# Performance work log

Hardware: AMD Instinct MI355X
Metric: run time of the kernel (lower is better)

## Reference

```python
import jax, jax.numpy as jnp
import numpy as np

D = 128      # embed_dim
H = 8        # num_heads
HD = D // H  # head_dim
TANH_CLIP = 10.0
B, N = 256, 2000


def setup_inputs() -> dict:
    key = jax.random.key(0)
    ks = jax.random.split(key, 16)
    node_embedding = jax.random.normal(ks[0], (B, N, D), jnp.float32)
    graph_embed = jax.random.normal(ks[1], (B, D), jnp.float32)
    h_last = jax.random.normal(ks[2], (B, D), jnp.float32)
    h_first = jax.random.normal(ks[3], (B, D), jnp.float32)
    visited_mask = jax.random.randint(ks[4], (B, N), 0, 2) > 0
    visited_mask = visited_mask.at[:, 0].set(False)  # keep >=1 valid key per row
    s = 1.0 / np.sqrt(D)
    v_l = jax.random.normal(ks[5], (1, D), jnp.float32)
    v_f = jax.random.normal(ks[6], (1, D), jnp.float32)
    w_q = jax.random.uniform(ks[7], (D, 3 * D), jnp.float32, -s, s)   # Linear(3D->D) weight [out,in]
    w_k = jax.random.uniform(ks[8], (D, D), jnp.float32, -s, s)
    w_v = jax.random.uniform(ks[9], (D, D), jnp.float32, -s, s)
    in_proj_w = jax.random.uniform(ks[10], (3 * D, D), jnp.float32, -s, s)  # MHA packed qkv proj
    in_proj_b = jnp.zeros((3 * D,), jnp.float32)
    out_w = jax.random.uniform(ks[11], (D, D), jnp.float32, -s, s)    # MHA out_proj weight
    out_b = jnp.zeros((D,), jnp.float32)
    return {
        'node_embedding': node_embedding, 'graph_embed': graph_embed,
        'h_last': h_last, 'h_first': h_first, 'visited_mask': visited_mask, 't': 1,
        'v_l': v_l, 'v_f': v_f, 'w_q': w_q, 'w_k': w_k, 'w_v': w_v,
        'in_proj_w': in_proj_w, 'in_proj_b': in_proj_b, 'out_w': out_w, 'out_b': out_b,
    }


def reference(node_embedding, graph_embed, h_last, h_first, visited_mask, t,
              v_l, v_f, w_q, w_k, w_v, in_proj_w, in_proj_b, out_w, out_b):
    b, n, d = node_embedding.shape
    if t == 0:  # static python int
        h_last = jnp.broadcast_to(v_l, (b, d))
        h_first = jnp.broadcast_to(v_f, (b, d))
    context = jnp.concatenate([graph_embed, h_last, h_first], axis=-1)  # [B,3D]

    q0 = context @ w_q.T                        # [B,D]
    k0 = jnp.einsum('bnd,ed->bne', node_embedding, w_k)  # [B,N,D]
    v0 = jnp.einsum('bnd,ed->bne', node_embedding, w_v)

    # nn.MultiheadAttention internal projections (packed in_proj)
    wq_i, wk_i, wv_i = in_proj_w[:d], in_proj_w[d:2 * d], in_proj_w[2 * d:]
    bq, bk, bv = in_proj_b[:d], in_proj_b[d:2 * d], in_proj_b[2 * d:]
    qp = (q0 @ wq_i.T + bq).reshape(b, H, HD)                 # single query
    kp = (jnp.einsum('bnd,ed->bne', k0, wk_i) + bk).reshape(b, n, H, HD)
    vp = (jnp.einsum('bnd,ed->bne', v0, wv_i) + bv).reshape(b, n, H, HD)

    scores = jnp.einsum('bhe,bnhe->bhn', qp, kp) / np.sqrt(HD)  # [B,H,N]
    scores = jnp.where(visited_mask[:, None, :], -jnp.inf, scores)
    attn = jax.nn.softmax(scores, axis=-1)
    ctx = jnp.einsum('bhn,bnhe->bhe', attn, vp).reshape(b, d)
    h_c_new = ctx @ out_w.T + out_b                           # [B,D]

    logits = jnp.einsum('bd,bnd->bn', h_c_new, k0) / np.sqrt(d)
    logits = TANH_CLIP * jnp.tanh(logits)
    logits = jnp.where(visited_mask, -jnp.inf, logits)
    probs = jax.nn.softmax(logits, axis=-1)
    return probs, logits
```

## Files before the change

kernel.cpp:

```cpp
#include <hip/hip_runtime.h>
#include <math.h>

#define DD 128
#define HH 8
#define BB 256
#define NNODES 2000
#define NSL 16
#define SLEN 125
#define CH 8
#define NCH 16
#define TANH_CLIPF 10.0f
#define NEG_BIG -1e30f

#define WS_WKP   0
#define WS_WVP   16384
#define WS_QH    32768
#define WS_QB    294912
#define WS_PM    296960
#define WS_PS    329728
#define WS_PACC  362496
#define WS_G     4556800
#define WS_LL    4589568

__global__ void prep_weights(const float* __restrict__ w_k, const float* __restrict__ w_v,
                             const float* __restrict__ in_proj_w, float* __restrict__ ws) {
    int idx = blockIdx.x * 256 + threadIdx.x;
    int mat = idx >> 14;
    int e = (idx >> 7) & 127;
    int d = idx & 127;
    const float* A  = in_proj_w + (mat ? 2 * DD * DD : DD * DD) + e * DD;
    const float* Bm = mat ? w_v : w_k;
    float acc = 0.f;
    for (int c = 0; c < DD; ++c) acc += A[c] * Bm[c * DD + d];
    ws[(mat ? WS_WVP : WS_WKP) + e * DD + d] = acc;
}

__global__ void prep_query(const float* __restrict__ graph_embed, const float* __restrict__ h_last,
                           const float* __restrict__ h_first, const int* __restrict__ t_ptr,
                           const float* __restrict__ v_l, const float* __restrict__ v_f,
                           const float* __restrict__ w_q, const float* __restrict__ in_proj_w,
                           const float* __restrict__ in_proj_b, float* __restrict__ ws) {
    __shared__ float ctx[3 * DD];
    __shared__ float q0[DD];
    __shared__ float qp[DD];
    int b = blockIdx.x, t = threadIdx.x;
    int t0 = t_ptr[0];
    for (int j = t; j < 3 * DD; j += 128) {
        float v;
        if (j < DD)           v = graph_embed[b * DD + j];
        else if (j < 2 * DD)  v = (t0 == 0) ? v_l[j - DD]     : h_last[b * DD + j - DD];
        else                  v = (t0 == 0) ? v_f[j - 2 * DD] : h_first[b * DD + j - 2 * DD];
        ctx[j] = v;
    }
    __syncthreads();
    {
        float a = 0.f;
        const float* wr = w_q + (size_t)t * 3 * DD;
        for (int j = 0; j < 3 * DD; ++j) a += ctx[j] * wr[j];
        q0[t] = a;
    }
    __syncthreads();
    {
        float a = in_proj_b[t];
        const float* wr = in_proj_w + (size_t)t * DD;
        for (int c = 0; c < DD; ++c) a += q0[c] * wr[c];
        qp[t] = a;
    }
    __syncthreads();
    const float inv = 0.25f;
    float* Qh = ws + WS_QH + (size_t)b * (HH * DD);
    for (int h = 0; h < HH; ++h) {
        float a = 0.f;
        for (int e = 0; e < 16; ++e) a += qp[h * 16 + e] * ws[WS_WKP + (h * 16 + e) * DD + t];
        Qh[h * DD + t] = a * inv;
    }
    if (t < HH) {
        float a = 0.f;
        for (int e = 0; e < 16; ++e) a += qp[t * 16 + e] * in_proj_b[DD + t * 16 + e];
        ws[WS_QB + b * HH + t] = a * inv;
    }
}

__global__ __launch_bounds__(256, 4) void attn_pass(const float* __restrict__ node,
                                                    const int* __restrict__ visited,
                                                    float* __restrict__ ws) {
    __shared__ float lds[4][CH * DD];
    int b    = blockIdx.x >> 2;
    int wq   = blockIdx.x & 3;
    int wave = threadIdx.x >> 6;
    int lane = threadIdx.x & 63;
    int sl   = wq * 4 + wave;
    int n0   = sl * SLEN;
    int c = lane >> 3, h = lane & 7;
    float* buf = lds[wave];

    const float* nb = node + (size_t)b * NNODES * DD;

    float4 qf0, qf1, qf2, qf3;
    {
        const float* qp = ws + WS_QH + (size_t)b * (HH * DD) + h * DD + c * 16;
        qf0 = *(const float4*)(qp + 0);
        qf1 = *(const float4*)(qp + 4);
        qf2 = *(const float4*)(qp + 8);
        qf3 = *(const float4*)(qp + 12);
    }
    float qb = ws[WS_QB + b * HH + h];

    const int* vb = visited + (size_t)b * NNODES;
    int vis0 = vb[n0 + (lane < SLEN ? lane : SLEN - 1)];
    int vis1 = vb[n0 + (lane + 64 < SLEN ? lane + 64 : SLEN - 1)];

    const int rsw0 = ((0 ^ ((c >> 1) & 3)) << 2);
    const int rsw1 = ((1 ^ ((c >> 1) & 3)) << 2);
    const int rsw2 = ((2 ^ ((c >> 1) & 3)) << 2);
    const int rsw3 = ((3 ^ ((c >> 1) & 3)) << 2);
    const int rbase = c * 16;

    const int srow = lane >> 3, scw = lane & 7;
    const int wb = srow * DD + scw * 16;
    const int wsw0 = ((0 ^ ((scw >> 1) & 3)) << 2);
    const int wsw1 = ((1 ^ ((scw >> 1) & 3)) << 2);
    const int wsw2 = ((2 ^ ((scw >> 1) & 3)) << 2);
    const int wsw3 = ((3 ^ ((scw >> 1) & 3)) << 2);

    float4 st0, st1, st2, st3;
    {
        int n = n0 + srow; if (n > NNODES - 1) n = NNODES - 1;
        const float* p = nb + (size_t)n * DD + scw * 16;
        st0 = *(const float4*)(p + 0); st1 = *(const float4*)(p + 4);
        st2 = *(const float4*)(p + 8); st3 = *(const float4*)(p + 12);
    }

    float m_h = NEG_BIG, s_h = 0.f;
    float4 a0 = make_float4(0.f,0.f,0.f,0.f), a1 = a0, a2 = a0, a3 = a0;

    for (int i = 0; i < NCH; ++i) {
        *(float4*)(buf + wb + wsw0) = st0;
        *(float4*)(buf + wb + wsw1) = st1;
        *(float4*)(buf + wb + wsw2) = st2;
        *(float4*)(buf + wb + wsw3) = st3;
        if (i + 1 < NCH) {
            int n = n0 + (i + 1) * CH + srow; if (n > NNODES - 1) n = NNODES - 1;
            const float* p = nb + (size_t)n * DD + scw * 16;
            st0 = *(const float4*)(p + 0); st1 = *(const float4*)(p + 4);
            st2 = *(const float4*)(p + 8); st3 = *(const float4*)(p + 12);
        }
        asm volatile("s_waitcnt lgkmcnt(0)" ::: "memory");
        __builtin_amdgcn_sched_barrier(0);

#define SCORE_N(n, dst) { \
            const float* rp = buf + (n) * DD + rbase; \
            float4 f0 = *(const float4*)(rp + rsw0); \
            float4 f1 = *(const float4*)(rp + rsw1); \
            float4 f2 = *(const float4*)(rp + rsw2); \
            float4 f3 = *(const float4*)(rp + rsw3); \
            dst = f0.x*qf0.x + f0.y*qf0.y + f0.z*qf0.z + f0.w*qf0.w \
                + f1.x*qf1.x + f1.y*qf1.y + f1.z*qf1.z + f1.w*qf1.w \
                + f2.x*qf2.x + f2.y*qf2.y + f2.z*qf2.z + f2.w*qf2.w \
                + f3.x*qf3.x + f3.y*qf3.y + f3.z*qf3.z + f3.w*qf3.w; }
        float v0,v1,v2,v3,v4,v5,v6,v7;
        SCORE_N(0, v0) SCORE_N(1, v1) SCORE_N(2, v2) SCORE_N(3, v3)
        SCORE_N(4, v4) SCORE_N(5, v5) SCORE_N(6, v6) SCORE_N(7, v7)
#undef SCORE_N

        float t0 = __shfl_xor(v0, 8, 64), t1 = __shfl_xor(v1, 8, 64);
        float t2 = __shfl_xor(v2, 8, 64), t3 = __shfl_xor(v3, 8, 64);
        float t4 = __shfl_xor(v4, 8, 64), t5 = __shfl_xor(v5, 8, 64);
        float t6 = __shfl_xor(v6, 8, 64), t7 = __shfl_xor(v7, 8, 64);
        int ck = c & 1;
        float u0 = ck ? (v1 + t1) : (v0 + t0);
        float u1 = ck ? (v3 + t3) : (v2 + t2);
        float u2 = ck ? (v5 + t5) : (v4 + t4);
        float u3 = ck ? (v7 + t7) : (v6 + t6);
        float s0 = __shfl_xor(u0, 16, 64), s1 = __shfl_xor(u1, 16, 64);
        float s2 = __shfl_xor(u2, 16, 64), s3 = __shfl_xor(u3, 16, 64);
        ck = (c >> 1) & 1;
        float w0 = ck ? (u1 + s1) : (u0 + s0);
        float w1 = ck ? (u3 + s3) : (u2 + s2);
        float r0 = __shfl_xor(w0, 32, 64), r1 = __shfl_xor(w1, 32, 64);
        ck = (c >> 2) & 1;
        float dotv = ck ? (w1 + r1) : (w0 + r0);

        int nidx = i * CH + c;
        int vlow  = __shfl(vis0, nidx & 63, 64);
        int vhigh = __shfl(vis1, nidx & 63, 64);
        int vv = (nidx < 64) ? vlow : vhigh;
        bool maskd = (nidx >= SLEN) || (vv != 0);
        float sc = maskd ? NEG_BIG : (dotv + qb);

        float mx = sc;
        mx = fmaxf(mx, __shfl_xor(mx, 8, 64));
        mx = fmaxf(mx, __shfl_xor(mx, 16, 64));
        mx = fmaxf(mx, __shfl_xor(mx, 32, 64));
        float m_new = fmaxf(m_h, mx);
        float p = (sc <= -1e29f) ? 0.f : expf(sc - m_new);
        float ps = p;
        ps += __shfl_xor(ps, 8, 64);
        ps += __shfl_xor(ps, 16, 64);
        ps += __shfl_xor(ps, 32, 64);
        float scale = expf(m_h - m_new);
        s_h = s_h * scale + ps;
        m_h = m_new;
        a0.x *= scale; a0.y *= scale; a0.z *= scale; a0.w *= scale;
        a1.x *= scale; a1.y *= scale; a1.z *= scale; a1.w *= scale;
        a2.x *= scale; a2.y *= scale; a2.z *= scale; a2.w *= scale;
        a3.x *= scale; a3.y *= scale; a3.z *= scale; a3.w *= scale;

#pragma unroll
        for (int n = 0; n < CH; ++n) {
            float pn = __shfl(p, n * 8 + h, 64);
            const float* rp = buf + n * DD + rbase;
            float4 f0 = *(const float4*)(rp + rsw0);
            float4 f1 = *(const float4*)(rp + rsw1);
            float4 f2 = *(const float4*)(rp + rsw2);
            float4 f3 = *(const float4*)(rp + rsw3);
            a0.x += pn * f0.x; a0.y += pn * f0.y; a0.z += pn * f0.z; a0.w += pn * f0.w;
            a1.x += pn * f1.x; a1.y += pn * f1.y; a1.z += pn * f1.z; a1.w += pn * f1.w;
            a2.x += pn * f2.x; a2.y += pn * f2.y; a2.z += pn * f2.z; a2.w += pn * f2.w;
            a3.x += pn * f3.x; a3.y += pn * f3.y; a3.z += pn * f3.z; a3.w += pn * f3.w;
        }
        __builtin_amdgcn_sched_barrier(0);
    }

    size_t pb = WS_PACC + (size_t)((b * NSL + sl) * HH + h) * DD + c * 16;
    *(float4*)(ws + pb + 0)  = a0;
    *(float4*)(ws + pb + 4)  = a1;
    *(float4*)(ws + pb + 8)  = a2;
    *(float4*)(ws + pb + 12) = a3;
    if (c == 0) {
        ws[WS_PM + (b * NSL + sl) * HH + h] = m_h;
        ws[WS_PS + (b * NSL + sl) * HH + h] = s_h;
    }
}

__global__ void merge_kernel(const float* __restrict__ in_proj_b, const float* __restrict__ out_w,
                             const float* __restrict__ out_b, const float* __restrict__ w_k,
                             float* __restrict__ ws) {
    __shared__ float cn[HH][132];
    __shared__ float ctxv[DD];
    __shared__ float hc[DD];
    __shared__ float Mh[HH], Sh[HH];
    int b = blockIdx.x, t = threadIdx.x;
    if (t < HH) {
        float M = NEG_BIG;
        for (int i = 0; i < NSL; ++i) M = fmaxf(M, ws[WS_PM + (b * NSL + i) * HH + t]);
        float stot = 0.f;
        for (int i = 0; i < NSL; ++i) {
            float s = ws[WS_PS + (b * NSL + i) * HH + t];
            float m = ws[WS_PM + (b * NSL + i) * HH + t];
            stot += (s > 0.f) ? expf(m - M) * s : 0.f;
        }
        Mh[t] = M; Sh[t] = stot;
    }
    __syncthreads();
    for (int h = 0; h < HH; ++h) {
        float a = 0.f;
        for (int i = 0; i < NSL; ++i) {
            float m = ws[WS_PM + (b * NSL + i) * HH + h];
            float s = ws[WS_PS + (b * NSL + i) * HH + h];
            float w = (s > 0.f) ? expf(m - Mh[h]) : 0.f;
            a += w * ws[WS_PACC + (size_t)((b * NSL + i) * HH + h) * DD + t];
        }
        cn[h][t] = a / Sh[h];
    }
    __syncthreads();
    {
        int h = t >> 4;
        float a = in_proj_b[2 * DD + t];
        const float* wv = ws + WS_WVP + (size_t)t * DD;
        for (int d = 0; d < DD; ++d) a += cn[h][d] * wv[d];
        ctxv[t] = a;
    }
    __syncthreads();
    {
        float a = out_b[t];
        const float* wr = out_w + (size_t)t * DD;
        for (int c = 0; c < DD; ++c) a += ctxv[c] * wr[c];
        hc[t] = a;
    }
    __syncthreads();
    {
        const float invd = 0.08838834764831845f;
        float a = 0.f;
        for (int e = 0; e < DD; ++e) a += hc[e] * w_k[e * DD + t];
        ws[WS_G + b * DD + t] = a * invd;
    }
}

__global__ __launch_bounds__(256, 8) void logits_ll(const float* __restrict__ node,
                                                    const int* __restrict__ visited,
                                                    float* __restrict__ ws) {
    int b = blockIdx.x >> 3, seg = blockIdx.x & 7;
    int wave = threadIdx.x >> 6, lane = threadIdx.x & 63;
    int r8 = lane >> 3, g = lane & 7;
    int base = seg * 250;
    const float* nb = node + (size_t)b * NNODES * DD;
    float4 g0, g1, g2, g3;
    {
        const float* gp = ws + WS_G + b * DD + g * 16;
        g0 = *(const float4*)(gp + 0); g1 = *(const float4*)(gp + 4);
        g2 = *(const float4*)(gp + 8); g3 = *(const float4*)(gp + 12);
    }
    float4 c0, c1, c2, c3;
    {
        int n = base + wave * 8 + r8;
        const float* p = nb + (size_t)n * DD + g * 16;
        c0 = *(const float4*)(p + 0); c1 = *(const float4*)(p + 4);
        c2 = *(const float4*)(p + 8); c3 = *(const float4*)(p + 12);
    }
    for (int it = 0; it < 8; ++it) {
        int rl = it * 32 + wave * 8 + r8;
        int row = base + rl;
        float4 n0 = c0, n1 = c1, n2 = c2, n3 = c3;
        if (it + 1 < 8) {
            int nr = base + (it + 1) * 32 + wave * 8 + r8;
            if (nr > NNODES - 1) nr = NNODES - 1;
            const float* p = nb + (size_t)nr * DD + g * 16;
            c0 = *(const float4*)(p + 0); c1 = *(const float4*)(p + 4);
            c2 = *(const float4*)(p + 8); c3 = *(const float4*)(p + 12);
        }
        float a = n0.x*g0.x + n0.y*g0.y + n0.z*g0.z + n0.w*g0.w
                + n1.x*g1.x + n1.y*g1.y + n1.z*g1.z + n1.w*g1.w
                + n2.x*g2.x + n2.y*g2.y + n2.z*g2.z + n2.w*g2.w
                + n3.x*g3.x + n3.y*g3.y + n3.z*g3.z + n3.w*g3.w;
        a += __shfl_xor(a, 1, 64);
        a += __shfl_xor(a, 2, 64);
        a += __shfl_xor(a, 4, 64);
        float val = TANH_CLIPF * tanhf(a);
        if (g == 0 && rl < 250) {
            if (visited[(size_t)b * NNODES + row]) val = NEG_BIG;
            ws[WS_LL + (size_t)b * NNODES + row] = val;
        }
    }
}

__global__ __launch_bounds__(256, 4) void softmax_out(const float* __restrict__ ws,
                                                      float* __restrict__ out) {
    __shared__ float red[4];
    int b = blockIdx.x, t = threadIdx.x;
    const float* ll = ws + WS_LL + (size_t)b * NNODES;
    float v0[8];
#pragma unroll
    for (int j = 0; j < 8; ++j) {
        int idx = j * 256 + t;
        v0[j] = (idx < NNODES) ? ll[idx] : NEG_BIG;
    }
    float mx = v0[0];
#pragma unroll
    for (int j = 1; j < 8; ++j) mx = fmaxf(mx, v0[j]);
    for (int m = 1; m <= 32; m <<= 1) mx = fmaxf(mx, __shfl_xor(mx, m, 64));
    int wv = t >> 6;
    if ((t & 63) == 0) red[wv] = mx;
    __syncthreads();
    float M = fmaxf(fmaxf(red[0], red[1]), fmaxf(red[2], red[3]));
    __syncthreads();
    float e[8]; float sm = 0.f;
#pragma unroll
    for (int j = 0; j < 8; ++j) { e[j] = expf(v0[j] - M); sm += e[j]; }
    for (int m = 1; m <= 32; m <<= 1) sm += __shfl_xor(sm, m, 64);
    if ((t & 63) == 0) red[wv] = sm;
    __syncthreads();
    float inv = 1.0f / (red[0] + red[1] + red[2] + red[3]);
#pragma unroll
    for (int j = 0; j < 8; ++j) {
        int idx = j * 256 + t;
        if (idx < NNODES) {
            out[(size_t)b * NNODES + idx] = e[j] * inv;
            out[(size_t)BB * NNODES + (size_t)b * NNODES + idx] = v0[j];
        }
    }
}

extern "C" void kernel_launch(void* const* d_in, const int* in_sizes, int n_in,
                              void* d_out, int out_size, void* d_ws, size_t ws_size,
                              hipStream_t stream) {
    const float* node        = (const float*)d_in[0];
    const float* graph_embed = (const float*)d_in[1];
    const float* h_last      = (const float*)d_in[2];
    const float* h_first     = (const float*)d_in[3];
    const int*   visited     = (const int*)d_in[4];
    const int*   t_ptr       = (const int*)d_in[5];
    const float* v_l         = (const float*)d_in[6];
    const float* v_f         = (const float*)d_in[7];
    const float* w_q         = (const float*)d_in[8];
    const float* w_k         = (const float*)d_in[9];
    const float* w_v         = (const float*)d_in[10];
    const float* in_proj_w   = (const float*)d_in[11];
    const float* in_proj_b   = (const float*)d_in[12];
    const float* out_w       = (const float*)d_in[13];
    const float* out_b       = (const float*)d_in[14];
    float* out = (float*)d_out;
    float* ws  = (float*)d_ws;

    prep_weights<<<128, 256, 0, stream>>>(w_k, w_v, in_proj_w, ws);
    prep_query<<<BB, 128, 0, stream>>>(graph_embed, h_last, h_first, t_ptr, v_l, v_f,
                                       w_q, in_proj_w, in_proj_b, ws);
    attn_pass<<<BB * 4, 256, 0, stream>>>(node, visited, ws);
    merge_kernel<<<BB, 128, 0, stream>>>(in_proj_b, out_w, out_b, w_k, ws);
    logits_ll<<<BB * 8, 256, 0, stream>>>(node, visited, ws);
    softmax_out<<<BB, 256, 0, stream>>>(ws, out);
}
```

Measured before the change: 496.5 us.

## Stream node rows directly from global memory, dropping LDS staging in attention pass

The attention pass no longer stages 8-node chunks in LDS with swizzled layouts. Each wave now walks its 125 nodes one at a time, with every lane loading interleaved float4 columns straight from global memory and prefetching the next row. The visited mask becomes a per-wave ballot bitmask. This removes LDS traffic, the swizzle bookkeeping and the chunk-level shuffle reduction. In exchange it runs a serial per-node online softmax with three shuffles and two expf per node, so the loop has far less parallelism per iteration and a longer dependency chain.

Result: slower. 517.4 us (+4.2%).

```diff
diff --git a/kernel.cpp b/kernel.cpp
--- a/kernel.cpp
+++ b/kernel.cpp
@@ -7,8 +7,6 @@
 #define NNODES 2000
 #define NSL 16
 #define SLEN 125
-#define CH 8
-#define NCH 16
 #define TANH_CLIPF 10.0f
 #define NEG_BIG -1e30f
 
@@ -84,7 +82,6 @@
 __global__ __launch_bounds__(256, 4) void attn_pass(const float* __restrict__ node,
                                                     const int* __restrict__ visited,
                                                     float* __restrict__ ws) {
-    __shared__ float lds[4][CH * DD];
     int b    = blockIdx.x >> 2;
     int wq   = blockIdx.x & 3;
     int wave = threadIdx.x >> 6;
@@ -92,141 +89,77 @@
     int sl   = wq * 4 + wave;
     int n0   = sl * SLEN;
     int c = lane >> 3, h = lane & 7;
-    float* buf = lds[wave];
 
     const float* nb = node + (size_t)b * NNODES * DD;
 
     float4 qf0, qf1, qf2, qf3;
     {
-        const float* qp = ws + WS_QH + (size_t)b * (HH * DD) + h * DD + c * 16;
-        qf0 = *(const float4*)(qp + 0);
-        qf1 = *(const float4*)(qp + 4);
-        qf2 = *(const float4*)(qp + 8);
-        qf3 = *(const float4*)(qp + 12);
+        const float* qp = ws + WS_QH + (size_t)b * (HH * DD) + h * DD;
+        qf0 = *(const float4*)(qp + (0 * 8 + c) * 4);
+        qf1 = *(const float4*)(qp + (1 * 8 + c) * 4);
+        qf2 = *(const float4*)(qp + (2 * 8 + c) * 4);
+        qf3 = *(const float4*)(qp + (3 * 8 + c) * 4);
     }
     float qb = ws[WS_QB + b * HH + h];
 
     const int* vb = visited + (size_t)b * NNODES;
-    int vis0 = vb[n0 + (lane < SLEN ? lane : SLEN - 1)];
-    int vis1 = vb[n0 + (lane + 64 < SLEN ? lane + 64 : SLEN - 1)];
-
-    const int rsw0 = ((0 ^ ((c >> 1) & 3)) << 2);
-    const int rsw1 = ((1 ^ ((c >> 1) & 3)) << 2);
-    const int rsw2 = ((2 ^ ((c >> 1) & 3)) << 2);
-    const int rsw3 = ((3 ^ ((c >> 1) & 3)) << 2);
-    const int rbase = c * 16;
-
-    const int srow = lane >> 3, scw = lane & 7;
-    const int wb = srow * DD + scw * 16;
-    const int wsw0 = ((0 ^ ((scw >> 1) & 3)) << 2);
-    const int wsw1 = ((1 ^ ((scw >> 1) & 3)) << 2);
-    const int wsw2 = ((2 ^ ((scw >> 1) & 3)) << 2);
-    const int wsw3 = ((3 ^ ((scw >> 1) & 3)) << 2);
-
-    float4 st0, st1, st2, st3;
-    {
-        int n = n0 + srow; if (n > NNODES - 1) n = NNODES - 1;
-        const float* p = nb + (size_t)n * DD + scw * 16;
-        st0 = *(const float4*)(p + 0); st1 = *(const float4*)(p + 4);
-        st2 = *(const float4*)(p + 8); st3 = *(const float4*)(p + 12);
-    }
+    int i1 = lane + 64 < SLEN ? lane + 64 : SLEN - 1;
+    unsigned long long mask0 = __ballot(vb[n0 + lane] != 0);
+    unsigned long long mask1 = __ballot(vb[n0 + i1] != 0);
 
     float m_h = NEG_BIG, s_h = 0.f;
-    float4 a0 = make_float4(0.f,0.f,0.f,0.f), a1 = a0, a2 = a0, a3 = a0;
-
-    for (int i = 0; i < NCH; ++i) {
-        *(float4*)(buf + wb + wsw0) = st0;
-        *(float4*)(buf + wb + wsw1) = st1;
-        *(float4*)(buf + wb + wsw2) = st2;
-        *(float4*)(buf + wb + wsw3) = st3;
-        if (i + 1 < NCH) {
-            int n = n0 + (i + 1) * CH + srow; if (n > NNODES - 1) n = NNODES - 1;
-            const float* p = nb + (size_t)n * DD + scw * 16;
-            st0 = *(const float4*)(p + 0); st1 = *(const float4*)(p + 4);
-            st2 = *(const float4*)(p + 8); st3 = *(const float4*)(p + 12);
-        }
-        asm volatile("s_waitcnt lgkmcnt(0)" ::: "memory");
-        __builtin_amdgcn_sched_barrier(0);
-
-#define SCORE_N(n, dst) { \
-            const float* rp = buf + (n) * DD + rbase; \
-            float4 f0 = *(const float4*)(rp + rsw0); \
-            float4 f1 = *(const float4*)(rp + rsw1); \
-            float4 f2 = *(const float4*)(rp + rsw2); \
-            float4 f3 = *(const float4*)(rp + rsw3); \
-            dst = f0.x*qf0.x + f0.y*qf0.y + f0.z*qf0.z + f0.w*qf0.w \
-                + f1.x*qf1.x + f1.y*qf1.y + f1.z*qf1.z + f1.w*qf1.w \
-                + f2.x*qf2.x + f2.y*qf2.y + f2.z*qf2.z + f2.w*qf2.w \
-                + f3.x*qf3.x + f3.y*qf3.y + f3.z*qf3.z + f3.w*qf3.w; }
-        float v0,v1,v2,v3,v4,v5,v6,v7;
-        SCORE_N(0, v0) SCORE_N(1, v1) SCORE_N(2, v2) SCORE_N(3, v3)
-        SCORE_N(4, v4) SCORE_N(5, v5) SCORE_N(6, v6) SCORE_N(7, v7)
-#undef SCORE_N
-
-        float t0 = __shfl_xor(v0, 8, 64), t1 = __shfl_xor(v1, 8, 64);
-        float t2 = __shfl_xor(v2, 8, 64), t3 = __shfl_xor(v3, 8, 64);
-        float t4 = __shfl_xor(v4, 8, 64), t5 = __shfl_xor(v5, 8, 64);
-        float t6 = __shfl_xor(v6, 8, 64), t7 = __shfl_xor(v7, 8, 64);
-        int ck = c & 1;
-        float u0 = ck ? (v1 + t1) : (v0 + t0);
-        float u1 = ck ? (v3 + t3) : (v2 + t2);
-        float u2 = ck ? (v5 + t5) : (v4 + t4);
-        float u3 = ck ? (v7 + t7) : (v6 + t6);
-        float s0 = __shfl_xor(u0, 16, 64), s1 = __shfl_xor(u1, 16, 64);
-        float s2 = __shfl_xor(u2, 16, 64), s3 = __shfl_xor(u3, 16, 64);
-        ck = (c >> 1) & 1;
-        float w0 = ck ? (u1 + s1) : (u0 + s0);
-        float w1 = ck ? (u3 + s3) : (u2 + s2);
-        float r0 = __shfl_xor(w0, 32, 64), r1 = __shfl_xor(w1, 32, 64);
-        ck = (c >> 2) & 1;
-        float dotv = ck ? (w1 + r1) : (w0 + r0);
-
-        int nidx = i * CH + c;
-        int vlow  = __shfl(vis0, nidx & 63, 64);
-        int vhigh = __shfl(vis1, nidx & 63, 64);
-        int vv = (nidx < 64) ? vlow : vhigh;
-        bool maskd = (nidx >= SLEN) || (vv != 0);
-        float sc = maskd ? NEG_BIG : (dotv + qb);
-
-        float mx = sc;
-        mx = fmaxf(mx, __shfl_xor(mx, 8, 64));
-        mx = fmaxf(mx, __shfl_xor(mx, 16, 64));
-        mx = fmaxf(mx, __shfl_xor(mx, 32, 64));
-        float m_new = fmaxf(m_h, mx);
-        float p = (sc <= -1e29f) ? 0.f : expf(sc - m_new);
-        float ps = p;
-        ps += __shfl_xor(ps, 8, 64);
-        ps += __shfl_xor(ps, 16, 64);
-        ps += __shfl_xor(ps, 32, 64);
+    float4 a0 = make_float4(0.f, 0.f, 0.f, 0.f), a1 = a0, a2 = a0, a3 = a0;
+
+    float4 A0, A1, A2, A3;
+    {
+        const float* rp = nb + (size_t)n0 * DD;
+        A0 = *(const float4*)(rp + (0 * 8 + c) * 4);
+        A1 = *(const float4*)(rp + (1 * 8 + c) * 4);
+        A2 = *(const float4*)(rp + (2 * 8 + c) * 4);
+        A3 = *(const float4*)(rp + (3 * 8 + c) * 4);
+    }
+
+    for (int n = 0; n < SLEN; ++n) {
+        float4 B0 = A0, B1 = A1, B2 = A2, B3 = A3;
+        if (n + 1 < SLEN) {
+            const float* rp = nb + (size_t)(n0 + n + 1) * DD;
+            B0 = *(const float4*)(rp + (0 * 8 + c) * 4);
+            B1 = *(const float4*)(rp + (1 * 8 + c) * 4);
+            B2 = *(const float4*)(rp + (2 * 8 + c) * 4);
+            B3 = *(const float4*)(rp + (3 * 8 + c) * 4);
+        }
+        float part = A0.x*qf0.x + A0.y*qf0.y + A0.z*qf0.z + A0.w*qf0.w
+                   + A1.x*qf1.x + A1.y*qf1.y + A1.z*qf1.z + A1.w*qf1.w
+                   + A2.x*qf2.x + A2.y*qf2.y + A2.z*qf2.z + A2.w*qf2.w
+                   + A3.x*qf3.x + A3.y*qf3.y + A3.z*qf3.z + A3.w*qf3.w;
+        part += __shfl_xor(part, 8, 64);
+        part += __shfl_xor(part, 16, 64);
+        part += __shfl_xor(part, 32, 64);
+
+        bool msk = (((n < 64 ? mask0 : mask1) >> (n & 63)) & 1ULL) != 0;
+        float sc = msk ? NEG_BIG : (part + qb);
+        float m_new = fmaxf(m_h, sc);
+        float p = msk ? 0.f : expf(sc - m_new);
         float scale = expf(m_h - m_new);
-        s_h = s_h * scale + ps;
+        s_h = s_h * scale + p;
         m_h = m_new;
-        a0.x *= scale; a0.y *= scale; a0.z *= scale; a0.w *= scale;
-        a1.x *= scale; a1.y *= scale; a1.z *= scale; a1.w *= scale;
-        a2.x *= scale; a2.y *= scale; a2.z *= scale; a2.w *= scale;
-        a3.x *= scale; a3.y *= scale; a3.z *= scale; a3.w *= scale;
-
-#pragma unroll
-        for (int n = 0; n < CH; ++n) {
-            float pn = __shfl(p, n * 8 + h, 64);
-            const float* rp = buf + n * DD + rbase;
-            float4 f0 = *(const float4*)(rp + rsw0);
-            float4 f1 = *(const float4*)(rp + rsw1);
-            float4 f2 = *(const float4*)(rp + rsw2);
-            float4 f3 = *(const float4*)(rp + rsw3);
-            a0.x += pn * f0.x; a0.y += pn * f0.y; a0.z += pn * f0.z; a0.w += pn * f0.w;
-            a1.x += pn * f1.x; a1.y += pn * f1.y; a1.z += pn * f1.z; a1.w += pn * f1.w;
-            a2.x += pn * f2.x; a2.y += pn * f2.y; a2.z += pn * f2.z; a2.w += pn * f2.w;
-            a3.x += pn * f3.x; a3.y += pn * f3.y; a3.z += pn * f3.z; a3.w += pn * f3.w;
-        }
-        __builtin_amdgcn_sched_barrier(0);
-    }
-
-    size_t pb = WS_PACC + (size_t)((b * NSL + sl) * HH + h) * DD + c * 16;
-    *(float4*)(ws + pb + 0)  = a0;
-    *(float4*)(ws + pb + 4)  = a1;
-    *(float4*)(ws + pb + 8)  = a2;
-    *(float4*)(ws + pb + 12) = a3;
+        a0.x = a0.x * scale + p * A0.x; a0.y = a0.y * scale + p * A0.y;
+        a0.z = a0.z * scale + p * A0.z; a0.w = a0.w * scale + p * A0.w;
+        a1.x = a1.x * scale + p * A1.x; a1.y = a1.y * scale + p * A1.y;
+        a1.z = a1.z * scale + p * A1.z; a1.w = a1.w * scale + p * A1.w;
+        a2.x = a2.x * scale + p * A2.x; a2.y = a2.y * scale + p * A2.y;
+        a2.z = a2.z * scale + p * A2.z; a2.w = a2.w * scale + p * A2.w;
+        a3.x = a3.x * scale + p * A3.x; a3.y = a3.y * scale + p * A3.y;
+        a3.z = a3.z * scale + p * A3.z; a3.w = a3.w * scale + p * A3.w;
+
+        A0 = B0; A1 = B1; A2 = B2; A3 = B3;
+    }
+
+    float* pb = ws + WS_PACC + (size_t)((b * NSL + sl) * HH + h) * DD;
+    *(float4*)(pb + (0 * 8 + c) * 4) = a0;
+    *(float4*)(pb + (1 * 8 + c) * 4) = a1;
+    *(float4*)(pb + (2 * 8 + c) * 4) = a2;
+    *(float4*)(pb + (3 * 8 + c) * 4) = a3;
     if (c == 0) {
         ws[WS_PM + (b * NSL + sl) * HH + h] = m_h;
         ws[WS_PS + (b * NSL + sl) * HH + h] = s_h;
```
